# Kernel tuning notes

Hardware: AMD Instinct MI355X
Metric: run time of the kernel (lower is better)

## Reference

```python
import jax, jax.numpy as jnp
import numpy as np

NUM_HEADS = 16
LN_EPS = 1e-5


def setup_inputs() -> dict:
    key = jax.random.key(0)
    ks = jax.random.split(key, 6)
    B, N, D = 4, 4096, 1024
    s = 1.0 / np.sqrt(D)
    return {
        "x": jax.random.normal(ks[0], (B, N, D), dtype=jnp.float32),
        "Wq": jax.random.normal(ks[1], (D, D), dtype=jnp.float32) * s,
        "Wk": jax.random.normal(ks[2], (D, D), dtype=jnp.float32) * s,
        "Wv": jax.random.normal(ks[3], (D, D), dtype=jnp.float32) * s,
        "Wo": jax.random.normal(ks[4], (D, D), dtype=jnp.float32) * s,
        "bo": jnp.zeros((D,), dtype=jnp.float32),
        "alpha": jax.random.uniform(ks[5], (1,), dtype=jnp.float32),
        "temperature": jnp.float32(1.0),
        "gamma": jnp.ones((D,), dtype=jnp.float32),
        "beta": jnp.zeros((D,), dtype=jnp.float32),
    }


def _layernorm(x, gamma, beta):
    mu = jnp.mean(x, axis=-1, keepdims=True)
    var = jnp.var(x, axis=-1, keepdims=True)
    return (x - mu) * jax.lax.rsqrt(var + LN_EPS) * gamma + beta


def reference(x, Wq, Wk, Wv, Wo, bo, alpha, temperature, gamma, beta):
    B, N, D = x.shape
    H = NUM_HEADS
    hd = D // H
    residual = x
    # projections (query=None -> query comes from x), nn.Linear: x @ W.T
    q = (x @ Wq.T).reshape(B, N, H, hd).transpose(0, 2, 1, 3)  # [B,H,N,hd]
    k = (x @ Wk.T).reshape(B, N, H, hd).transpose(0, 2, 1, 3)
    v = (x @ Wv.T).reshape(B, N, H, hd).transpose(0, 2, 1, 3)
    # kk = K^T K + alpha*I, per (batch, head): [B,H,hd,hd]
    kk = jnp.einsum('bhnd,bhne->bhde', k, k)
    kk = kk + alpha[0] * jnp.eye(hd, dtype=x.dtype)
    kk_inv = jnp.linalg.inv(kk)
    # attn_map = kk_inv @ K^T @ V : [B,H,hd,hd]
    ktv = jnp.einsum('bhnd,bhne->bhde', k, v)
    attn_map = kk_inv @ ktv
    attn_map = jax.nn.softmax(attn_map / temperature, axis=-2)
    out = q @ attn_map  # [B,H,N,hd]
    out = out.transpose(0, 2, 1, 3).reshape(B, N, D)
    out = out @ Wo.T + bo
    return _layernorm(out + residual, gamma, beta)
```

## Files before the change

### kernel.cpp

```cpp
#include <hip/hip_runtime.h>
#include <cstdint>
#include <cstddef>

typedef unsigned short u16;
typedef __bf16 bf16x8 __attribute__((ext_vector_type(8)));
typedef float f32x4 __attribute__((ext_vector_type(4)));
typedef u16 u16x8 __attribute__((ext_vector_type(8)));
typedef u16 u16x4 __attribute__((ext_vector_type(4)));

#define NB 4
#define NN 4096
#define ND 1024
#define NH 16
#define NTOK (NB * NN)

__device__ __forceinline__ u16 f2bf(float f) {
    unsigned u = __float_as_uint(f);
    u += 0x7fffu + ((u >> 16) & 1u);
    return (u16)(u >> 16);
}

__device__ __forceinline__ void gload_lds16(const void* g, void* l) {
    __builtin_amdgcn_global_load_lds(
        (const __attribute__((address_space(1))) void*)g,
        (__attribute__((address_space(3))) void*)l, 16, 0, 0);
}

__global__ __launch_bounds__(256) void prep_cast(
    const float* __restrict__ x,
    const float* __restrict__ wq, const float* __restrict__ wk,
    const float* __restrict__ wv, const float* __restrict__ wo,
    u16* __restrict__ xb, u16* __restrict__ wb)
{
    const int n_x4 = (NTOK * ND) / 4;
    const int n_w4 = (ND * ND) / 4;
    const int total = n_x4 + 4 * n_w4;
    for (int i = blockIdx.x * blockDim.x + threadIdx.x; i < total;
         i += gridDim.x * blockDim.x) {
        float4 v;
        u16* dst;
        if (i < n_x4) {
            v = ((const float4*)x)[i];
            dst = xb + (size_t)i * 4;
        } else {
            int j = i - n_x4;
            int w = j / n_w4;
            int off = j - w * n_w4;
            const float* src = (w == 0) ? wq : (w == 1) ? wk : (w == 2) ? wv : wo;
            v = ((const float4*)src)[off];
            dst = wb + (size_t)j * 4;
        }
        u16x4 o;
        o[0] = f2bf(v.x); o[1] = f2bf(v.y); o[2] = f2bf(v.z); o[3] = f2bf(v.w);
        *(u16x4*)dst = o;
    }
}

template <int OUT_MODE>
__global__ __launch_bounds__(256, 2) void gemm_bt(
    const u16* __restrict__ A, int lda,
    const u16* __restrict__ Bw, int ldb,
    void* __restrict__ Cout, int ldc, int K,
    const float* __restrict__ bias, const float* __restrict__ resid,
    int rows_per_batch, size_t b_stride)
{
    __shared__ alignas(16) u16 lA[256 * 64];
    __shared__ alignas(16) u16 lB[128 * 64];

    const int tid = threadIdx.x;
    const int wv = tid >> 6, lane = tid & 63;
    const int quad = lane >> 4, lrow = lane & 15;
    const int row0 = blockIdx.y * 256, col0 = blockIdx.x * 128;
    const int wm = (wv >> 1) * 128, wn = (wv & 1) * 64;

    const u16* Bp = Bw + (b_stride ? (size_t)(row0 / rows_per_batch) * b_stride : 0);

    f32x4 acc[8][4] = {};

    const int srow = lane >> 3;
    const int cswE = ((lane & 7) ^ srow) * 8;

    for (int k0 = 0; k0 < K; k0 += 64) {
        __syncthreads();
#pragma unroll
        for (int i = 0; i < 8; ++i) {
            int rb = wv * 64 + i * 8;
            gload_lds16(A + (size_t)(row0 + rb + srow) * lda + k0 + cswE,
                        &lA[rb * 64]);
        }
#pragma unroll
        for (int i = 0; i < 4; ++i) {
            int rb = wv * 32 + i * 8;
            gload_lds16(Bp + (size_t)(col0 + rb + srow) * ldb + k0 + cswE,
                        &lB[rb * 64]);
        }
        __syncthreads();

#pragma unroll
        for (int kc = 0; kc < 2; ++kc) {
            const int ch = ((kc * 4 + quad) ^ (lrow & 7)) * 8;
            bf16x8 bfv[4];
#pragma unroll
            for (int t = 0; t < 4; ++t)
                bfv[t] = *(const bf16x8*)&lB[(wn + t * 16 + lrow) * 64 + ch];
#pragma unroll
            for (int mt = 0; mt < 8; ++mt) {
                bf16x8 af = *(const bf16x8*)&lA[(wm + mt * 16 + lrow) * 64 + ch];
#pragma unroll
                for (int nt = 0; nt < 4; ++nt)
                    acc[mt][nt] = __builtin_amdgcn_mfma_f32_16x16x32_bf16(
                        af, bfv[nt], acc[mt][nt], 0, 0, 0);
            }
        }
    }

    float bvals[4];
    if (OUT_MODE == 1) {
#pragma unroll
        for (int nt = 0; nt < 4; ++nt)
            bvals[nt] = bias[col0 + wn + nt * 16 + lrow];
    }
#pragma unroll
    for (int mt = 0; mt < 8; ++mt)
#pragma unroll
        for (int nt = 0; nt < 4; ++nt)
#pragma unroll
            for (int r = 0; r < 4; ++r) {
                int grow = row0 + wm + mt * 16 + quad * 4 + r;
                int gcol = col0 + wn + nt * 16 + lrow;
                if (OUT_MODE == 0) {
                    ((u16*)Cout)[(size_t)grow * ldc + gcol] = f2bf(acc[mt][nt][r]);
                } else {
                    float vv = acc[mt][nt][r] + bvals[nt] +
                               resid[(size_t)grow * ldc + gcol];
                    ((float*)Cout)[(size_t)grow * ldc + gcol] = vv;
                }
            }
}

__global__ __launch_bounds__(256) void stage2a_kernel(
    const u16* __restrict__ qkv,
    float* __restrict__ Part)
{
    __shared__ alignas(16) u16 sKt[4][64][40];
    __shared__ alignas(16) u16 sVt[4][64][40];
    __shared__ float S[64][132];

    const int tid = threadIdx.x;
    const int wv = tid >> 6, lane = tid & 63;
    const int quad = lane >> 4, lrow = lane & 15;
    const int bh = blockIdx.x, split = blockIdx.y;
    const int b = bh >> 4, h = bh & 15;

    f32x4 akk[4][4] = {};
    f32x4 aktv[4][4] = {};
    const u16* kbase = qkv + ND + h * 64;
    const u16* vbase = qkv + 2 * ND + h * 64;
    const size_t tok0 = (size_t)b * NN;

    for (int it = 0; it < 2; ++it) {
        const int n0 = split * 256 + wv * 64 + it * 32;
#pragma unroll
        for (int pass = 0; pass < 4; ++pass) {
            int nl = pass * 8 + (lane >> 3);
            int d0 = (lane & 7) * 8;
            size_t roff = (tok0 + n0 + nl) * 3072 + d0;
            u16x8 kvv = *(const u16x8*)(kbase + roff);
            u16x8 vvv = *(const u16x8*)(vbase + roff);
#pragma unroll
            for (int j = 0; j < 8; ++j) {
                sKt[wv][d0 + j][nl] = kvv[j];
                sVt[wv][d0 + j][nl] = vvv[j];
            }
        }
        bf16x8 fK[4], fV[4];
#pragma unroll
        for (int t = 0; t < 4; ++t) {
            fK[t] = *(const bf16x8*)&sKt[wv][t * 16 + lrow][quad * 8];
            fV[t] = *(const bf16x8*)&sVt[wv][t * 16 + lrow][quad * 8];
        }
#pragma unroll
        for (int mt = 0; mt < 4; ++mt)
#pragma unroll
            for (int et = 0; et < 4; ++et) {
                akk[mt][et] = __builtin_amdgcn_mfma_f32_16x16x32_bf16(
                    fK[mt], fK[et], akk[mt][et], 0, 0, 0);
                aktv[mt][et] = __builtin_amdgcn_mfma_f32_16x16x32_bf16(
                    fK[mt], fV[et], aktv[mt][et], 0, 0, 0);
            }
    }

    for (int w = 0; w < 4; ++w) {
        if (wv == w) {
#pragma unroll
            for (int mt = 0; mt < 4; ++mt)
#pragma unroll
                for (int et = 0; et < 4; ++et)
#pragma unroll
                    for (int r = 0; r < 4; ++r) {
                        int row = mt * 16 + quad * 4 + r;
                        int col = et * 16 + lrow;
                        if (w == 0) {
                            S[row][col] = akk[mt][et][r];
                            S[row][64 + col] = aktv[mt][et][r];
                        } else {
                            S[row][col] += akk[mt][et][r];
                            S[row][64 + col] += aktv[mt][et][r];
                        }
                    }
        }
        __syncthreads();
    }

    float* dst = Part + (size_t)(bh * 16 + split) * 8192;
#pragma unroll
    for (int c = 0; c < 8; ++c) {
        int idx = tid * 4 + c * 1024;
        int row = idx >> 7, col = idx & 127;
        float4 v = *(const float4*)&S[row][col];
        ((float4*)dst)[idx >> 2] = v;
    }
}

__global__ __launch_bounds__(256) void stage2b_kernel(
    const float* __restrict__ Part,
    const u16* __restrict__ wb,
    const float* __restrict__ alpha,
    const float* __restrict__ temp,
    u16* __restrict__ Mout)
{
    __shared__ float S[64][132];
    __shared__ float colbuf[2][64];
    __shared__ alignas(16) u16 sAttn[64][72];

    const int tid = threadIdx.x;
    const int wv = tid >> 6, lane = tid & 63;
    const int quad = lane >> 4, lrow = lane & 15;
    const int b = blockIdx.x >> 4, h = blockIdx.x & 15;

    const float* Pb = Part + (size_t)blockIdx.x * 16 * 8192;
#pragma unroll
    for (int c = 0; c < 8; ++c) {
        int idx = tid * 4 + c * 1024;
        float4 a = ((const float4*)Pb)[idx >> 2];
#pragma unroll
        for (int s = 1; s < 16; ++s) {
            float4 t4 = ((const float4*)(Pb + (size_t)s * 8192))[idx >> 2];
            a.x += t4.x; a.y += t4.y; a.z += t4.z; a.w += t4.w;
        }
        int row = idx >> 7, col = idx & 127;
        *(float4*)&S[row][col] = a;
    }
    __syncthreads();

    const float aval = alpha[0];
    const int c0 = wv * 32;
    float R[32];
#pragma unroll
    for (int j = 0; j < 32; ++j) {
        R[j] = S[lane][c0 + j];
        if (c0 + j == lane) R[j] += aval;
    }
    if (wv == 0) colbuf[0][lane] = R[0];
    __syncthreads();

    float mydiag = 1.0f;
    for (int p = 0; p < 64; ++p) {
        const int cur = p & 1;
        float cv = colbuf[cur][lane];
        float pv = colbuf[cur][p];
        if (p == lane) mydiag = pv;
        float m = (lane == p) ? 0.0f : cv * __builtin_amdgcn_rcpf(pv);
#pragma unroll
        for (int j = 0; j < 32; ++j) {
            float rowv = __uint_as_float(
                __builtin_amdgcn_readlane(__float_as_uint(R[j]), p));
            R[j] -= m * rowv;
        }
        if (p < 63) {
            int pn = p + 1;
            if (wv == (pn >> 5)) colbuf[cur ^ 1][lane] = R[pn & 31];
        }
        __syncthreads();
    }

    if (wv >= 2) {
        const float idg = __builtin_amdgcn_rcpf(mydiag) * (1.0f / temp[0]);
#pragma unroll
        for (int j = 0; j < 32; ++j) {
            float xv = R[j] * idg;
            float mx = xv;
#pragma unroll
            for (int off = 32; off > 0; off >>= 1)
                mx = fmaxf(mx, __shfl_xor(mx, off, 64));
            float ev = __expf(xv - mx);
            float sum = ev;
#pragma unroll
            for (int off = 32; off > 0; off >>= 1)
                sum += __shfl_xor(sum, off, 64);
            sAttn[lane][(wv - 2) * 32 + j] = f2bf(ev * __builtin_amdgcn_rcpf(sum));
        }
    }
    __syncthreads();

    {
        bf16x8 fB[4][2];
#pragma unroll
        for (int nt = 0; nt < 4; ++nt)
#pragma unroll
            for (int ks = 0; ks < 2; ++ks)
                fB[nt][ks] = *(const bf16x8*)&sAttn[nt * 16 + lrow][ks * 32 + quad * 8];

        const u16* wo = wb + (size_t)3072 * ND + h * 64;
        u16* Mb = Mout + (size_t)b * ND * ND + h * 64;
        for (int i = 0; i < 16; ++i) {
            int mt = wv * 16 + i;
            int oA = mt * 16 + lrow;
            bf16x8 fA[2];
#pragma unroll
            for (int ks = 0; ks < 2; ++ks)
                fA[ks] = *(const bf16x8*)(wo + (size_t)oA * ND + ks * 32 + quad * 8);
#pragma unroll
            for (int nt = 0; nt < 4; ++nt) {
                f32x4 acc = {};
                acc = __builtin_amdgcn_mfma_f32_16x16x32_bf16(fA[0], fB[nt][0], acc, 0, 0, 0);
                acc = __builtin_amdgcn_mfma_f32_16x16x32_bf16(fA[1], fB[nt][1], acc, 0, 0, 0);
#pragma unroll
                for (int r = 0; r < 4; ++r) {
                    int o = mt * 16 + quad * 4 + r;
                    Mb[(size_t)o * ND + nt * 16 + lrow] = f2bf(acc[r]);
                }
            }
        }
    }
}

__global__ __launch_bounds__(256) void ln_kernel(
    const float* __restrict__ y, const float* __restrict__ gamma,
    const float* __restrict__ beta, float* __restrict__ out)
{
    const int row = blockIdx.x, tid = threadIdx.x;
    const float4 v = ((const float4*)(y + (size_t)row * ND))[tid];
    float s = v.x + v.y + v.z + v.w;
    float q = v.x * v.x + v.y * v.y + v.z * v.z + v.w * v.w;
#pragma unroll
    for (int off = 32; off > 0; off >>= 1) {
        s += __shfl_xor(s, off, 64);
        q += __shfl_xor(q, off, 64);
    }
    __shared__ float ss[4], sq[4];
    const int wv = tid >> 6;
    if ((tid & 63) == 0) { ss[wv] = s; sq[wv] = q; }
    __syncthreads();
    s = ss[0] + ss[1] + ss[2] + ss[3];
    q = sq[0] + sq[1] + sq[2] + sq[3];
    const float mu = s * (1.0f / ND);
    const float var = q * (1.0f / ND) - mu * mu;
    const float rs = rsqrtf(var + 1e-5f);
    const float4 g = ((const float4*)gamma)[tid];
    const float4 bt = ((const float4*)beta)[tid];
    float4 o;
    o.x = (v.x - mu) * rs * g.x + bt.x;
    o.y = (v.y - mu) * rs * g.y + bt.y;
    o.z = (v.z - mu) * rs * g.z + bt.z;
    o.w = (v.w - mu) * rs * g.w + bt.w;
    ((float4*)(out + (size_t)row * ND))[tid] = o;
}

extern "C" void kernel_launch(void* const* d_in, const int* in_sizes, int n_in,
                              void* d_out, int out_size, void* d_ws, size_t ws_size,
                              hipStream_t stream)
{
    const float* x     = (const float*)d_in[0];
    const float* Wq    = (const float*)d_in[1];
    const float* Wk    = (const float*)d_in[2];
    const float* Wv    = (const float*)d_in[3];
    const float* Wo    = (const float*)d_in[4];
    const float* bo    = (const float*)d_in[5];
    const float* alpha = (const float*)d_in[6];
    const float* temp  = (const float*)d_in[7];
    const float* gamma = (const float*)d_in[8];
    const float* beta  = (const float*)d_in[9];

    char* ws = (char*)d_ws;
    u16* xb   = (u16*)(ws);
    float* Part = (float*)(ws);
    u16* wb   = (u16*)(ws + 33554432);
    u16* qkv  = (u16*)(ws + 41943040);
    u16* Mb   = (u16*)(ws + 142606336);
    float* y  = (float*)(ws + 150994944);
    float* out = (float*)d_out;

    prep_cast<<<dim3(4096), dim3(256), 0, stream>>>(x, Wq, Wk, Wv, Wo, xb, wb);

    gemm_bt<0><<<dim3(24, 64), dim3(256), 0, stream>>>(
        xb, 1024, wb, 1024, (void*)qkv, 3072, 1024,
        nullptr, nullptr, 1 << 30, (size_t)0);

    stage2a_kernel<<<dim3(64, 16), dim3(256), 0, stream>>>(qkv, Part);
    stage2b_kernel<<<dim3(64), dim3(256), 0, stream>>>(Part, wb, alpha, temp, Mb);

    gemm_bt<1><<<dim3(8, 64), dim3(256), 0, stream>>>(
        qkv, 3072, Mb, 1024, (void*)y, 1024, 1024,
        bo, x, 4096, (size_t)(1024 * 1024));

    ln_kernel<<<dim3(16384), dim3(256), 0, stream>>>(y, gamma, beta, out);
}
```

Before: 414.6 us.

## Double-buffer GEMM LDS tiles with 256x256 blocks, 8 waves and XCD remap

Rewrites the bf16 GEMM to use 512-thread workgroups computing 256x256 tiles, with double-buffered LDS loads so global-to-LDS copies of the next K-slice overlap MFMA work on the current one. It adds a workgroup-id remap that groups blocks across XCDs, plus barrier and priority hints around the MFMA clusters. This aims to hide memory latency and improve operand reuse per block. In exchange LDS use grows to 128KB per block and the grid has fewer blocks, which may limit occupancy.

```diff
diff --git a/kernel.cpp b/kernel.cpp
--- a/kernel.cpp
+++ b/kernel.cpp
@@ -57,81 +57,144 @@
 }
 
 template <int OUT_MODE>
-__global__ __launch_bounds__(256, 2) void gemm_bt(
+__global__ __launch_bounds__(512, 2) void gemm_bt(
     const u16* __restrict__ A, int lda,
     const u16* __restrict__ Bw, int ldb,
     void* __restrict__ Cout, int ldc, int K,
     const float* __restrict__ bias, const float* __restrict__ resid,
     int rows_per_batch, size_t b_stride)
 {
-    __shared__ alignas(16) u16 lA[256 * 64];
-    __shared__ alignas(16) u16 lB[128 * 64];
+    __shared__ alignas(16) u16 lA[2][256 * 64];
+    __shared__ alignas(16) u16 lB[2][256 * 64];
 
     const int tid = threadIdx.x;
     const int wv = tid >> 6, lane = tid & 63;
     const int quad = lane >> 4, lrow = lane & 15;
-    const int row0 = blockIdx.y * 256, col0 = blockIdx.x * 128;
-    const int wm = (wv >> 1) * 128, wn = (wv & 1) * 64;
+
+    const int nwg = gridDim.x * gridDim.y;
+    const int orig = blockIdx.y * gridDim.x + blockIdx.x;
+    const int cpx = nwg >> 3;
+    const int wgid = (orig & 7) * cpx + (orig >> 3);
+    const int bx = wgid % gridDim.x;
+    const int by = wgid / gridDim.x;
+
+    const int row0 = by * 256, col0 = bx * 256;
+    const int wm = wv >> 2, wn = wv & 3;
 
     const u16* Bp = Bw + (b_stride ? (size_t)(row0 / rows_per_batch) * b_stride : 0);
-
-    f32x4 acc[8][4] = {};
 
     const int srow = lane >> 3;
     const int cswE = ((lane & 7) ^ srow) * 8;
 
-    for (int k0 = 0; k0 < K; k0 += 64) {
-        __syncthreads();
-#pragma unroll
-        for (int i = 0; i < 8; ++i) {
-            int rb = wv * 64 + i * 8;
+    f32x4 acc[8][4] = {};
+
+    auto stage = [&](u16* dA, u16* dB, int k0) {
+#pragma unroll
+        for (int i = 0; i < 4; ++i) {
+            int rb = wv * 32 + i * 8;
             gload_lds16(A + (size_t)(row0 + rb + srow) * lda + k0 + cswE,
-                        &lA[rb * 64]);
+                        &dA[rb * 64]);
         }
 #pragma unroll
         for (int i = 0; i < 4; ++i) {
             int rb = wv * 32 + i * 8;
             gload_lds16(Bp + (size_t)(col0 + rb + srow) * ldb + k0 + cswE,
-                        &lB[rb * 64]);
-        }
-        __syncthreads();
-
+                        &dB[rb * 64]);
+        }
+    };
+
+    auto tile = [&](const u16* cA, const u16* cB) {
 #pragma unroll
         for (int kc = 0; kc < 2; ++kc) {
             const int ch = ((kc * 4 + quad) ^ (lrow & 7)) * 8;
             bf16x8 bfv[4];
 #pragma unroll
-            for (int t = 0; t < 4; ++t)
-                bfv[t] = *(const bf16x8*)&lB[(wn + t * 16 + lrow) * 64 + ch];
-#pragma unroll
-            for (int mt = 0; mt < 8; ++mt) {
-                bf16x8 af = *(const bf16x8*)&lA[(wm + mt * 16 + lrow) * 64 + ch];
-#pragma unroll
-                for (int nt = 0; nt < 4; ++nt)
-                    acc[mt][nt] = __builtin_amdgcn_mfma_f32_16x16x32_bf16(
-                        af, bfv[nt], acc[mt][nt], 0, 0, 0);
-            }
-        }
+            for (int n = 0; n < 4; ++n)
+                bfv[n] = *(const bf16x8*)&cB[(wn * 64 + n * 16 + lrow) * 64 + ch];
+            {
+                bf16x8 af[4];
+#pragma unroll
+                for (int m = 0; m < 4; ++m)
+                    af[m] = *(const bf16x8*)&cA[(wm * 128 + m * 16 + lrow) * 64 + ch];
+                __builtin_amdgcn_s_barrier();
+                asm volatile("s_waitcnt lgkmcnt(0)" ::: "memory");
+                __builtin_amdgcn_sched_barrier(0);
+                __builtin_amdgcn_s_setprio(1);
+#pragma unroll
+                for (int m = 0; m < 4; ++m)
+#pragma unroll
+                    for (int n = 0; n < 4; ++n)
+                        acc[m][n] = __builtin_amdgcn_mfma_f32_16x16x32_bf16(
+                            af[m], bfv[n], acc[m][n], 0, 0, 0);
+                __builtin_amdgcn_s_setprio(0);
+                __builtin_amdgcn_s_barrier();
+            }
+            {
+                bf16x8 ag[4];
+#pragma unroll
+                for (int m = 0; m < 4; ++m)
+                    ag[m] = *(const bf16x8*)&cA[(wm * 128 + (4 + m) * 16 + lrow) * 64 + ch];
+                __builtin_amdgcn_s_barrier();
+                asm volatile("s_waitcnt lgkmcnt(0)" ::: "memory");
+                __builtin_amdgcn_sched_barrier(0);
+                __builtin_amdgcn_s_setprio(1);
+#pragma unroll
+                for (int m = 0; m < 4; ++m)
+#pragma unroll
+                    for (int n = 0; n < 4; ++n)
+                        acc[4 + m][n] = __builtin_amdgcn_mfma_f32_16x16x32_bf16(
+                            ag[m], bfv[n], acc[4 + m][n], 0, 0, 0);
+                __builtin_amdgcn_s_setprio(0);
+                __builtin_amdgcn_s_barrier();
+            }
+        }
+    };
+
+    stage(lA[0], lB[0], 0);
+    stage(lA[1], lB[1], 64);
+    asm volatile("s_waitcnt vmcnt(8)" ::: "memory");
+    __builtin_amdgcn_s_barrier();
+
+    const int nt = K >> 6;
+#pragma unroll 1
+    for (int t = 0; t < nt; t += 2) {
+        tile(lA[0], lB[0]);
+        if (t + 2 < nt) {
+            stage(lA[0], lB[0], (t + 2) * 64);
+            asm volatile("s_waitcnt vmcnt(8)" ::: "memory");
+        } else {
+            asm volatile("s_waitcnt vmcnt(0)" ::: "memory");
+        }
+        __builtin_amdgcn_s_barrier();
+
+        tile(lA[1], lB[1]);
+        if (t + 3 < nt) {
+            stage(lA[1], lB[1], (t + 3) * 64);
+            asm volatile("s_waitcnt vmcnt(8)" ::: "memory");
+        } else {
+            asm volatile("s_waitcnt vmcnt(0)" ::: "memory");
+        }
+        __builtin_amdgcn_s_barrier();
     }
 
     float bvals[4];
     if (OUT_MODE == 1) {
 #pragma unroll
-        for (int nt = 0; nt < 4; ++nt)
-            bvals[nt] = bias[col0 + wn + nt * 16 + lrow];
+        for (int nt2 = 0; nt2 < 4; ++nt2)
+            bvals[nt2] = bias[col0 + wn * 64 + nt2 * 16 + lrow];
     }
 #pragma unroll
     for (int mt = 0; mt < 8; ++mt)
 #pragma unroll
-        for (int nt = 0; nt < 4; ++nt)
+        for (int nt2 = 0; nt2 < 4; ++nt2)
 #pragma unroll
             for (int r = 0; r < 4; ++r) {
-                int grow = row0 + wm + mt * 16 + quad * 4 + r;
-                int gcol = col0 + wn + nt * 16 + lrow;
+                int grow = row0 + wm * 128 + mt * 16 + quad * 4 + r;
+                int gcol = col0 + wn * 64 + nt2 * 16 + lrow;
                 if (OUT_MODE == 0) {
-                    ((u16*)Cout)[(size_t)grow * ldc + gcol] = f2bf(acc[mt][nt][r]);
+                    ((u16*)Cout)[(size_t)grow * ldc + gcol] = f2bf(acc[mt][nt2][r]);
                 } else {
-                    float vv = acc[mt][nt][r] + bvals[nt] +
+                    float vv = acc[mt][nt2][r] + bvals[nt2] +
                                resid[(size_t)grow * ldc + gcol];
                     ((float*)Cout)[(size_t)grow * ldc + gcol] = vv;
                 }
@@ -393,14 +456,14 @@
 
     prep_cast<<<dim3(4096), dim3(256), 0, stream>>>(x, Wq, Wk, Wv, Wo, xb, wb);
 
-    gemm_bt<0><<<dim3(24, 64), dim3(256), 0, stream>>>(
+    gemm_bt<0><<<dim3(12, 64), dim3(512), 0, stream>>>(
         xb, 1024, wb, 1024, (void*)qkv, 3072, 1024,
         nullptr, nullptr, 1 << 30, (size_t)0);
 
     stage2a_kernel<<<dim3(64, 16), dim3(256), 0, stream>>>(qkv, Part);
     stage2b_kernel<<<dim3(64), dim3(256), 0, stream>>>(Part, wb, alpha, temp, Mb);
 
-    gemm_bt<1><<<dim3(8, 64), dim3(256), 0, stream>>>(
+    gemm_bt<1><<<dim3(4, 64), dim3(512), 0, stream>>>(
         qkv, 3072, Mb, 1024, (void*)y, 1024, 1024,
         bo, x, 4096, (size_t)(1024 * 1024));
 
```

Measured after the change: 431.3 us. +4.0%, slower.
